# Kernel tuning notes

Hardware: AMD Instinct MI355X
Metric: run time of the kernel (lower is better)

The kernel has to match this reference:

```python
import jax, jax.numpy as jnp
import numpy as np

# Model dims (match init_kwargs)
L = 2048; B = 2; E = 1024; H = 16; NUM = 2; NG = 4; DG = 16
ODIM = E // H // NUM        # 32  origin_head_dim
DQK = ODIM * NG             # 128 qk_head_dim
QKD = DQK * H               # 2048 qk_dim
DV = E // H                 # 64  v_head_dim
EPS = 1e-12


def _one_mask(n, e, n_groups, step):
    """Faithful port of MultiheadSpluAttention.get_one_mask (numpy, setup-time only)."""
    e1 = e * n_groups
    mask = np.ones((n, e1))
    row_num = (e1 - e) // step + 1
    group1 = [list(range(i * step, i * step + e)) for i in range(row_num)]
    group2 = group1[::-1]
    group_index = [group1, group2]
    col_index = []
    l = n // row_num
    k = 0
    for i in range(l):
        for j in range(i * row_num, (i + 1) * row_num):
            col_index.append(group_index[k][j % row_num])
        k = 1 - k
    if n % row_num != 0:
        for j in range(l * row_num, n):
            col_index.append(group_index[k][j % row_num])
    mask[np.arange(n).reshape(-1, 1), np.array(col_index)] = 0
    return mask


def _build_masks(n):
    # head 0: no mask; heads 1..H-1 use step = head index
    ms = [np.zeros((n, DQK))]
    for s in range(1, H):
        ms.append(_one_mask(n, ODIM, NG, s))
    masks = np.stack(ms).astype(bool)            # (H, n, DQK); True = zero-out
    gmask = np.ones((n, DQK), dtype=bool)        # global: keep only first/last DG rows
    gmask[:DG, :] = False
    gmask[n - DG:, :] = False
    return jnp.asarray(masks), jnp.asarray(gmask)


def _xavier(key, shape, gain=1.0):
    fan_out, fan_in = shape
    a = gain * np.sqrt(6.0 / (fan_in + fan_out))
    return jax.random.uniform(key, shape, jnp.float32, -a, a)


def setup_inputs() -> dict:
    key = jax.random.key(0)
    ks = jax.random.split(key, 8)
    g = 1.0 / np.sqrt(2.0)
    masks, gmask = _build_masks(L)
    return {
        "query": jax.random.normal(ks[0], (L, B, E), jnp.float32),
        "key": jax.random.normal(ks[1], (L, B, E), jnp.float32),
        "value": jax.random.normal(ks[2], (L, B, E), jnp.float32),
        "Wq": _xavier(ks[3], (QKD, E), g), "bq": jnp.zeros((QKD,), jnp.float32),
        "Wk": _xavier(ks[4], (QKD, E), g), "bk": jnp.zeros((QKD,), jnp.float32),
        "Wv": _xavier(ks[5], (E, E), g),  "bv": jnp.zeros((E,), jnp.float32),
        "Wo": _xavier(ks[6], (E, E)),     "bo": jnp.zeros((E,), jnp.float32),
        "masks": masks,   # (H, L, DQK) bool
        "gmask": gmask,   # (L, DQK) bool
    }


def reference(query, key, value, Wq, bq, Wk, bk, Wv, bv, Wo, bo, masks, gmask):
    Lq, Bb, Ee = query.shape
    S = key.shape[0]
    Hh, _, dqk = masks.shape
    dv = Ee // Hh
    scaling = float(Wq.shape[0]) ** (-0.5)  # qk_dim ** -0.5

    q = jax.nn.relu(query @ Wq.T + bq) * scaling          # (L, B, QKD)
    k = jax.nn.relu(key @ Wk.T + bk)                       # (S, B, QKD)
    v = value @ Wv.T + bv                                  # (S, B, E)

    q = q.reshape(Lq, Bb, Hh, dqk).transpose(1, 2, 0, 3)   # (B, H, L, dqk)
    k = k.reshape(S, Bb, Hh, dqk).transpose(1, 2, 0, 3)    # (B, H, S, dqk)
    v = v.reshape(S, Bb, Hh, dv).transpose(1, 2, 0, 3)     # (B, H, S, dv)

    q1 = jnp.where(masks[None, :, :Lq], 0.0, q)            # per-head group mask
    k1 = jnp.where(masks[None, :, :S], 0.0, k)
    kg = jnp.where(gmask[None, None, :S], 0.0, k)          # keep only global tokens

    w = (jnp.einsum('bhld,bhsd->bhls', q1, k1)
         + jnp.einsum('bhld,bhsd->bhls', q, kg))           # (B, H, L, S)
    denom = jnp.maximum(jnp.sum(w, axis=-1, keepdims=True), EPS)
    w = w / denom                                          # relu-linear normalization

    out = jnp.einsum('bhls,bhsd->bhld', w, v)              # (B, H, L, dv)
    out = out.transpose(2, 0, 1, 3).reshape(Lq, Bb, Ee)    # (L, B, E)
    return out @ Wo.T + bo
```

## Files before the change

### kernel.cpp

```cpp
#include <hip/hip_runtime.h>

typedef unsigned short u16;
typedef __attribute__((ext_vector_type(8))) short s16x8;
typedef __attribute__((ext_vector_type(4))) float f32x4;

#define DEV static __device__ __forceinline__

#define CB 2
#define CM 4096
#define MBH 16640
#define OQ 0u
#define OK 4194304u
#define OV 8388608u
#define OWQ 12582912u
#define OWK 14680064u
#define OWV 16777216u
#define OWO 17825792u
#define SCALING 0.022097086912079608f

DEV float b2f(u16 u) { union { unsigned int i; float f; } x; x.i = (unsigned int)u << 16; return x.f; }
DEV u16 f2b(float f) {
  union { float f; unsigned int i; } x; x.f = f;
  unsigned int r = (x.i + 0x7FFFu + ((x.i >> 16) & 1u)) >> 16;
  return (u16)r;
}

DEV void async_cp16(const u16* g, u16* l) {
  __builtin_amdgcn_global_load_lds((__attribute__((address_space(1))) void*)g,
                                   (__attribute__((address_space(3))) void*)l,
                                   16, 0, 0);
}

#define MFMA16 __builtin_amdgcn_mfma_f32_16x16x32_bf16

__global__ void detect_stride(const unsigned char* __restrict__ m, int* __restrict__ flag) {
  if (threadIdx.x == 0) {
    const size_t base = (size_t)1 * 2048 * 128;
    int shift = 0;
    const int cands[3] = {0, 2, 3};
    for (int t = 0; t < 3; ++t) {
      int s = cands[t];
      bool ok = (m[(base + 100) << s] == 1) && (m[(base + 10) << s] == 0) &&
                (m[(base + 32) << s] == 1) && (m[(base + 31) << s] == 0);
      if (ok) { shift = s; break; }
    }
    *flag = shift;
  }
}

struct ConvDesc { const float* src; unsigned dst_off; unsigned n; };
struct ConvArgs { ConvDesc d[7]; };

__global__ __launch_bounds__(256) void convert_all(ConvArgs a, u16* __restrict__ dst_base) {
  ConvDesc dd = a.d[blockIdx.y];
  unsigned i = (blockIdx.x * 256u + threadIdx.x) * 4u;
  if (i >= dd.n) return;
  float4 v = *(const float4*)(dd.src + i);
  ushort4 p;
  p.x = f2b(v.x); p.y = f2b(v.y); p.z = f2b(v.z); p.w = f2b(v.w);
  *(ushort4*)(dst_base + dd.dst_off + i) = p;
}

__global__ __launch_bounds__(256) void gemm_qkv(const u16* __restrict__ cvt,
                                                const float* __restrict__ bq,
                                                const float* __restrict__ bk,
                                                const float* __restrict__ bv,
                                                u16* __restrict__ qbuf,
                                                u16* __restrict__ kbuf,
                                                u16* __restrict__ vbuf,
                                                u16* __restrict__ kg,
                                                const unsigned char* __restrict__ mb,
                                                const int* __restrict__ flag) {
  __shared__ u16 sA[128 * 64];
  __shared__ u16 sB[128 * 64];
  const int bx = blockIdx.x;

  const u16* A; const u16* W; const float* bias; u16* C;
  int N, nx; bool relu, domask; float scale;
  if (bx < 16) {
    A = cvt + OQ; W = cvt + OWQ; bias = bq; C = qbuf;
    N = 2048; nx = bx; relu = true; domask = false; scale = SCALING;
  } else if (bx < 32) {
    A = cvt + OK; W = cvt + OWK; bias = bk; C = kbuf;
    N = 2048; nx = bx - 16; relu = true; domask = true; scale = 1.0f;
  } else {
    A = cvt + OV; W = cvt + OWV; bias = bv; C = vbuf;
    N = 1024; nx = bx - 32; relu = false; domask = false; scale = 1.0f;
  }

  const int tid = threadIdx.x;
  const int lane = tid & 63;
  const int wv = tid >> 6;
  const int m0 = blockIdx.y * 128;
  const int n0 = nx * 128;

  const int rowi = lane >> 3;
  const int chk = lane & 7;
  const int lr = lane & 15;
  const int lq = lane >> 4;
  const int mq = (wv >> 1) * 64;
  const int nq = (wv & 1) * 64;

  const int shift = domask ? *flag : 0;

  f32x4 acc[4][4] = {};

  for (int k0 = 0; k0 < 1024; k0 += 64) {
#pragma unroll
    for (int i = 0; i < 4; ++i) {
      int t = wv * 4 + i;
      int row = t * 8 + rowi;
      async_cp16(A + (size_t)(m0 + row) * 1024 + k0 + chk * 8, sA + t * 512);
      async_cp16(W + (size_t)(n0 + row) * 1024 + k0 + chk * 8, sB + t * 512);
    }
    __syncthreads();
    s16x8 af[4][2], bfr[4][2];
#pragma unroll
    for (int mt = 0; mt < 4; ++mt) {
      af[mt][0] = *(const s16x8*)&sA[(mq + mt * 16 + lr) * 64 + lq * 8];
      af[mt][1] = *(const s16x8*)&sA[(mq + mt * 16 + lr) * 64 + 32 + lq * 8];
    }
#pragma unroll
    for (int nt = 0; nt < 4; ++nt) {
      bfr[nt][0] = *(const s16x8*)&sB[(nq + nt * 16 + lr) * 64 + lq * 8];
      bfr[nt][1] = *(const s16x8*)&sB[(nq + nt * 16 + lr) * 64 + 32 + lq * 8];
    }
#pragma unroll
    for (int kk = 0; kk < 2; ++kk)
#pragma unroll
      for (int mt = 0; mt < 4; ++mt)
#pragma unroll
        for (int nt = 0; nt < 4; ++nt)
          acc[mt][nt] = MFMA16(af[mt][kk], bfr[nt][kk], acc[mt][nt], 0, 0, 0);
    __syncthreads();
  }

#pragma unroll
  for (int mt = 0; mt < 4; ++mt) {
#pragma unroll
    for (int nt = 0; nt < 4; ++nt) {
      int col = n0 + nq + nt * 16 + lr;
      float bv_ = bias[col];
      size_t mcb = (size_t)(col >> 7) * 262144 + (col & 127);
#pragma unroll
      for (int r = 0; r < 4; ++r) {
        int row = m0 + mq + mt * 16 + lq * 4 + r;
        float x = acc[mt][nt][r] + bv_;
        if (relu) x = fmaxf(x, 0.0f);
        x *= scale;
        u16 vb = f2b(x);
        if (domask) {
          int s = row >> 1;
          u16 out = mb[(mcb + (size_t)s * 128) << shift] ? (u16)0 : vb;
          C[(size_t)row * N + col] = out;
          if (s < 16 || s >= 2032) {
            int gi = s < 16 ? s : s - 2016;
            kg[(size_t)((gi << 1) | (row & 1)) * 2048 + col] = vb;
          }
        } else {
          C[(size_t)row * N + col] = vb;
        }
      }
    }
  }
}

__global__ __launch_bounds__(256) void gemm_bt_f32(const u16* __restrict__ A,
                                                   const u16* __restrict__ W,
                                                   const float* __restrict__ bias,
                                                   float* __restrict__ Cp,
                                                   int M, int N, int K) {
  __shared__ u16 sA[128 * 64];
  __shared__ u16 sB[128 * 64];
  const int tid = threadIdx.x;
  const int lane = tid & 63;
  const int wv = tid >> 6;
  const int m0 = blockIdx.y * 128;
  const int n0 = blockIdx.x * 128;

  const int rowi = lane >> 3;
  const int chk = lane & 7;
  const int lr = lane & 15;
  const int lq = lane >> 4;
  const int mq = (wv >> 1) * 64;
  const int nq = (wv & 1) * 64;

  f32x4 acc[4][4] = {};

  for (int k0 = 0; k0 < K; k0 += 64) {
#pragma unroll
    for (int i = 0; i < 4; ++i) {
      int t = wv * 4 + i;
      int row = t * 8 + rowi;
      async_cp16(A + (size_t)(m0 + row) * K + k0 + chk * 8, sA + t * 512);
      async_cp16(W + (size_t)(n0 + row) * K + k0 + chk * 8, sB + t * 512);
    }
    __syncthreads();
    s16x8 af[4][2], bfr[4][2];
#pragma unroll
    for (int mt = 0; mt < 4; ++mt) {
      af[mt][0] = *(const s16x8*)&sA[(mq + mt * 16 + lr) * 64 + lq * 8];
      af[mt][1] = *(const s16x8*)&sA[(mq + mt * 16 + lr) * 64 + 32 + lq * 8];
    }
#pragma unroll
    for (int nt = 0; nt < 4; ++nt) {
      bfr[nt][0] = *(const s16x8*)&sB[(nq + nt * 16 + lr) * 64 + lq * 8];
      bfr[nt][1] = *(const s16x8*)&sB[(nq + nt * 16 + lr) * 64 + 32 + lq * 8];
    }
#pragma unroll
    for (int kk = 0; kk < 2; ++kk)
#pragma unroll
      for (int mt = 0; mt < 4; ++mt)
#pragma unroll
        for (int nt = 0; nt < 4; ++nt)
          acc[mt][nt] = MFMA16(af[mt][kk], bfr[nt][kk], acc[mt][nt], 0, 0, 0);
    __syncthreads();
  }

#pragma unroll
  for (int mt = 0; mt < 4; ++mt) {
#pragma unroll
    for (int nt = 0; nt < 4; ++nt) {
      int col = n0 + nq + nt * 16 + lr;
      float bv = bias[col];
#pragma unroll
      for (int r = 0; r < 4; ++r) {
        int row = m0 + mq + mt * 16 + lq * 4 + r;
        Cp[(size_t)row * N + col] = acc[mt][nt][r] + bv;
      }
    }
  }
}

__global__ __launch_bounds__(256) void build_m_mfma(const u16* __restrict__ kbuf,
                                                    const u16* __restrict__ vbuf,
                                                    const u16* __restrict__ kgbuf,
                                                    float* __restrict__ Mbuf) {
  __shared__ u16 sKr[32 * 128];
  __shared__ u16 sVr[32 * 64];
  const int tid = threadIdx.x;
  const int lane = tid & 63;
  const int wv = tid >> 6;
  const int lr = lane & 15;
  const int lq = lane >> 4;
  const int chunk = blockIdx.x;
  const int bh = blockIdx.y;
  const int b = bh >> 4, h = bh & 15;

  const int sA = wv * 4 + (lane >> 4);
  const int dA = (lane & 15) * 8;
  const int sV = wv * 8 + (lane >> 3);
  const int eV = (lane & 7) * 8;
  u16* dstK1 = sKr + wv * 512;
  u16* dstK2 = sKr + 2048 + wv * 512;
  u16* dstV = sVr + wv * 512;

  const s16x8 onesf = {0x3F80, 0x3F80, 0x3F80, 0x3F80, 0x3F80, 0x3F80, 0x3F80, 0x3F80};

  f32x4 acc[2][4] = {};
  f32x4 accm[2] = {};

  for (int ks = 0; ks < 8; ++ks) {
    const int s0 = chunk * 256 + ks * 32;
    async_cp16(kbuf + (size_t)((s0 + sA) * 2 + b) * 2048 + h * 128 + dA, dstK1);
    async_cp16(kbuf + (size_t)((s0 + 16 + sA) * 2 + b) * 2048 + h * 128 + dA, dstK2);
    async_cp16(vbuf + (size_t)((s0 + sV) * 2 + b) * 1024 + h * 64 + eV, dstV);
    __syncthreads();
    s16x8 A0, A1, B0, B1, B2, B3;
#pragma unroll
    for (int j = 0; j < 8; ++j) {
      const int sr = (lq * 8 + j) * 128;
      A0[j] = (short)sKr[sr + wv * 32 + lr];
      A1[j] = (short)sKr[sr + wv * 32 + 16 + lr];
      const int vr = (lq * 8 + j) * 64;
      B0[j] = (short)sVr[vr + lr];
      B1[j] = (short)sVr[vr + 16 + lr];
      B2[j] = (short)sVr[vr + 32 + lr];
      B3[j] = (short)sVr[vr + 48 + lr];
    }
    acc[0][0] = MFMA16(A0, B0, acc[0][0], 0, 0, 0);
    acc[0][1] = MFMA16(A0, B1, acc[0][1], 0, 0, 0);
    acc[0][2] = MFMA16(A0, B2, acc[0][2], 0, 0, 0);
    acc[0][3] = MFMA16(A0, B3, acc[0][3], 0, 0, 0);
    acc[1][0] = MFMA16(A1, B0, acc[1][0], 0, 0, 0);
    acc[1][1] = MFMA16(A1, B1, acc[1][1], 0, 0, 0);
    acc[1][2] = MFMA16(A1, B2, acc[1][2], 0, 0, 0);
    acc[1][3] = MFMA16(A1, B3, acc[1][3], 0, 0, 0);
    accm[0] = MFMA16(A0, onesf, accm[0], 0, 0, 0);
    accm[1] = MFMA16(A1, onesf, accm[1], 0, 0, 0);
    __syncthreads();
  }

  float* Mg = Mbuf + (size_t)bh * MBH;
#pragma unroll
  for (int dg = 0; dg < 2; ++dg) {
    const int dbase = wv * 32 + dg * 16 + lq * 4;
#pragma unroll
    for (int eg = 0; eg < 4; ++eg)
#pragma unroll
      for (int r = 0; r < 4; ++r)
        atomicAdd(&Mg[(size_t)(dbase + r) * 64 + eg * 16 + lr], acc[dg][eg][r]);
    if (lr == 0) {
#pragma unroll
      for (int r = 0; r < 4; ++r) atomicAdd(&Mg[16384 + dbase + r], accm[dg][r]);
    }
  }

  if (chunk == 0) {
    f32x4 acc2[2][4] = {};
    f32x4 accm2[2] = {};
    const int sVact = sV < 16 ? sV : 2016 + sV;
    async_cp16(kgbuf + (size_t)(sA * 2 + b) * 2048 + h * 128 + dA, dstK1);
    async_cp16(kgbuf + (size_t)((16 + sA) * 2 + b) * 2048 + h * 128 + dA, dstK2);
    async_cp16(vbuf + (size_t)(sVact * 2 + b) * 1024 + h * 64 + eV, dstV);
    __syncthreads();
    s16x8 A0, A1, B0, B1, B2, B3;
#pragma unroll
    for (int j = 0; j < 8; ++j) {
      const int sr = (lq * 8 + j) * 128;
      A0[j] = (short)sKr[sr + wv * 32 + lr];
      A1[j] = (short)sKr[sr + wv * 32 + 16 + lr];
      const int vr = (lq * 8 + j) * 64;
      B0[j] = (short)sVr[vr + lr];
      B1[j] = (short)sVr[vr + 16 + lr];
      B2[j] = (short)sVr[vr + 32 + lr];
      B3[j] = (short)sVr[vr + 48 + lr];
    }
    acc2[0][0] = MFMA16(A0, B0, acc2[0][0], 0, 0, 0);
    acc2[0][1] = MFMA16(A0, B1, acc2[0][1], 0, 0, 0);
    acc2[0][2] = MFMA16(A0, B2, acc2[0][2], 0, 0, 0);
    acc2[0][3] = MFMA16(A0, B3, acc2[0][3], 0, 0, 0);
    acc2[1][0] = MFMA16(A1, B0, acc2[1][0], 0, 0, 0);
    acc2[1][1] = MFMA16(A1, B1, acc2[1][1], 0, 0, 0);
    acc2[1][2] = MFMA16(A1, B2, acc2[1][2], 0, 0, 0);
    acc2[1][3] = MFMA16(A1, B3, acc2[1][3], 0, 0, 0);
    accm2[0] = MFMA16(A0, onesf, accm2[0], 0, 0, 0);
    accm2[1] = MFMA16(A1, onesf, accm2[1], 0, 0, 0);
#pragma unroll
    for (int dg = 0; dg < 2; ++dg) {
      const int dbase = wv * 32 + dg * 16 + lq * 4;
#pragma unroll
      for (int eg = 0; eg < 4; ++eg)
#pragma unroll
        for (int r = 0; r < 4; ++r)
          Mg[8192 + (size_t)(dbase + r) * 64 + eg * 16 + lr] = acc2[dg][eg][r];
      if (lr == 0) {
#pragma unroll
        for (int r = 0; r < 4; ++r) Mg[16512 + dbase + r] = accm2[dg][r];
      }
    }
  }
}

__global__ __launch_bounds__(128) void prep_m(const float* __restrict__ Mbuf,
                                              u16* __restrict__ Mp) {
  const int n = blockIdx.x;
  const int bh = blockIdx.y;
  const int d = threadIdx.x;
  const float* Mg = Mbuf + (size_t)bh * MBH;
  float v1 = 0.f, v2 = 0.f;
  if (n < 64) { v1 = Mg[d * 64 + n]; v2 = Mg[8192 + d * 64 + n]; }
  else if (n == 64) { v1 = Mg[16384 + d]; v2 = Mg[16512 + d]; }
  u16 h1 = f2b(v1); float l1 = v1 - b2f(h1);
  u16 h2 = f2b(v2); float l2 = v2 - b2f(h2);
  u16* dst = Mp + (size_t)bh * 40960;
  const int dsw = d ^ ((n & 7) << 3);
  dst[(0 * 80 + n) * 128 + dsw] = h1;
  dst[(1 * 80 + n) * 128 + dsw] = f2b(l1);
  dst[(2 * 80 + n) * 128 + dsw] = h2;
  dst[(3 * 80 + n) * 128 + dsw] = f2b(l2);
}

__global__ __launch_bounds__(256) void apply_mfma(const u16* __restrict__ qbuf,
                                                  const u16* __restrict__ Mp,
                                                  u16* __restrict__ attn,
                                                  const unsigned char* __restrict__ mb,
                                                  const int* __restrict__ flag) {
  __shared__ u16 sB[4 * 80 * 128];
  const int tid = threadIdx.x;
  const int lane = tid & 63;
  const int wv = tid >> 6;
  const int lr = lane & 15;
  const int lq = lane >> 4;
  const int bh = blockIdx.x;
  const int b = bh >> 4, h = bh & 15;
  const int l0 = blockIdx.y * 256;
  const int shift = *flag;

  {
    const u16* src = Mp + (size_t)bh * 40960;
#pragma unroll
    for (int i = 0; i < 20; ++i)
      async_cp16(src + (size_t)(i * 4 + wv) * 512 + lane * 8, sB + (i * 4 + wv) * 512);
  }
  __syncthreads();

  f32x4 acc[4][5] = {};
  const int lrow = l0 + wv * 64;

  for (int d0 = 0; d0 < 128; d0 += 32) {
    s16x8 aq[4], a1[4];
#pragma unroll
    for (int mt = 0; mt < 4; ++mt) {
      const int l = lrow + mt * 16 + lr;
      aq[mt] = *(const s16x8*)&qbuf[((size_t)(l * 2 + b)) * 2048 + h * 128 + d0 + lq * 8];
      const size_t mi = ((size_t)(h * 2048 + l)) * 128 + d0 + lq * 8;
      s16x8 t = aq[mt];
      if (shift == 0) {
        unsigned long long mm = *(const unsigned long long*)&mb[mi];
#pragma unroll
        for (int j = 0; j < 8; ++j)
          if ((mm >> (8 * j)) & 0xffull) t[j] = 0;
      } else {
#pragma unroll
        for (int j = 0; j < 8; ++j)
          if (mb[(mi + j) << shift]) t[j] = 0;
      }
      a1[mt] = t;
    }
    const int eb = (d0 >> 3) + lq;
#pragma unroll
    for (int nt = 0; nt < 5; ++nt) {
      const int n = nt * 16 + lr;
      const u16* bp = &sB[(size_t)n * 128 + ((eb ^ (n & 7)) << 3)];
      s16x8 b1h = *(const s16x8*)&bp[0];
      s16x8 b1l = *(const s16x8*)&bp[10240];
      s16x8 b2h = *(const s16x8*)&bp[20480];
      s16x8 b2l = *(const s16x8*)&bp[30720];
#pragma unroll
      for (int mt = 0; mt < 4; ++mt) {
        acc[mt][nt] = MFMA16(a1[mt], b1h, acc[mt][nt], 0, 0, 0);
        acc[mt][nt] = MFMA16(a1[mt], b1l, acc[mt][nt], 0, 0, 0);
        acc[mt][nt] = MFMA16(aq[mt], b2h, acc[mt][nt], 0, 0, 0);
        acc[mt][nt] = MFMA16(aq[mt], b2l, acc[mt][nt], 0, 0, 0);
      }
    }
  }

#pragma unroll
  for (int mt = 0; mt < 4; ++mt) {
#pragma unroll
    for (int r = 0; r < 4; ++r) {
      float den = __shfl(acc[mt][4][r], lane & 48);
      float inv = 1.0f / fmaxf(den, 1e-12f);
      const int row = lrow + mt * 16 + lq * 4 + r;
      u16* o = attn + ((size_t)(row * 2 + b)) * 1024 + h * 64;
#pragma unroll
      for (int nt = 0; nt < 4; ++nt)
        o[nt * 16 + lr] = f2b(acc[mt][nt][r] * inv);
    }
  }
}

extern "C" void kernel_launch(void* const* d_in, const int* in_sizes, int n_in,
                              void* d_out, int out_size, void* d_ws, size_t ws_size,
                              hipStream_t stream) {
  (void)in_sizes; (void)n_in; (void)out_size; (void)ws_size;

  const float* bq = (const float*)d_in[4];
  const float* bk = (const float*)d_in[6];
  const float* bv = (const float*)d_in[8];
  const float* bo = (const float*)d_in[10];
  const unsigned char* mbytes = (const unsigned char*)d_in[11];

  char* ws = (char*)d_ws;
  u16* qbuf = (u16*)ws;
  u16* kbuf = (u16*)(ws + 16777216);
  float* Mbuf = (float*)(ws + 33554432);
  int* flag = (int*)(ws + 35684352);
  u16* cvt = (u16*)(ws + 35684368);
  u16* vbuf = (u16*)d_out;
  u16* kgbuf = (u16*)((char*)d_out + 8388608);
  u16* Mprep = (u16*)d_out;
  u16* attn = kbuf;

  hipMemsetAsync(Mbuf, 0, 32 * MBH * sizeof(float), stream);
  detect_stride<<<dim3(1), dim3(64), 0, stream>>>(mbytes, flag);

  ConvArgs ca;
  ca.d[0] = {(const float*)d_in[0], OQ, 4194304u};
  ca.d[1] = {(const float*)d_in[1], OK, 4194304u};
  ca.d[2] = {(const float*)d_in[2], OV, 4194304u};
  ca.d[3] = {(const float*)d_in[3], OWQ, 2097152u};
  ca.d[4] = {(const float*)d_in[5], OWK, 2097152u};
  ca.d[5] = {(const float*)d_in[7], OWV, 1048576u};
  ca.d[6] = {(const float*)d_in[9], OWO, 1048576u};
  convert_all<<<dim3(4096, 7), dim3(256), 0, stream>>>(ca, cvt);

  dim3 blk(256);
  gemm_qkv<<<dim3(40, 32), blk, 0, stream>>>(cvt, bq, bk, bv, qbuf, kbuf, vbuf, kgbuf, mbytes, flag);
  build_m_mfma<<<dim3(8, 32), blk, 0, stream>>>(kbuf, vbuf, kgbuf, Mbuf);
  prep_m<<<dim3(80, 32), dim3(128), 0, stream>>>(Mbuf, Mprep);
  apply_mfma<<<dim3(32, 8), blk, 0, stream>>>(qbuf, Mprep, attn, mbytes, flag);
  gemm_bt_f32<<<dim3(8, 32), blk, 0, stream>>>(attn, cvt + OWO, bo, (float*)d_out, CM, 1024, 1024);
}
```

Baseline: 349.8 us.

## Rewrite QKV projection GEMM as 256x256 tiled, double-buffered, XOR-swizzled pipelined kernel

Replaces the 128x128 single-buffered QKV GEMM with a 512-thread kernel that computes 256x256 output tiles using eight waves. Shared-memory tiles are double-buffered and XOR-swizzled, and global loads for upcoming k-steps are interleaved with MFMA phases under fine-grained barriers and s_setprio. The goal is to hide load latency, avoid LDS bank conflicts and raise data reuse per load. In exchange there are fewer blocks (320), so the grid may fill the GPU less evenly, and register and LDS pressure goes up.

```diff
diff --git a/kernel.cpp b/kernel.cpp
--- a/kernel.cpp
+++ b/kernel.cpp
@@ -61,104 +61,135 @@
   *(ushort4*)(dst_base + dd.dst_off + i) = p;
 }
 
-__global__ __launch_bounds__(256) void gemm_qkv(const u16* __restrict__ cvt,
-                                                const float* __restrict__ bq,
-                                                const float* __restrict__ bk,
-                                                const float* __restrict__ bv,
-                                                u16* __restrict__ qbuf,
-                                                u16* __restrict__ kbuf,
-                                                u16* __restrict__ vbuf,
-                                                u16* __restrict__ kg,
-                                                const unsigned char* __restrict__ mb,
-                                                const int* __restrict__ flag) {
-  __shared__ u16 sA[128 * 64];
-  __shared__ u16 sB[128 * 64];
+__global__ __launch_bounds__(512, 2) void gemm_qkv8(const u16* __restrict__ cvt,
+                                                    const float* __restrict__ bq,
+                                                    const float* __restrict__ bk,
+                                                    const float* __restrict__ bv,
+                                                    u16* __restrict__ qbuf,
+                                                    u16* __restrict__ kbuf,
+                                                    u16* __restrict__ vbuf,
+                                                    u16* __restrict__ kg,
+                                                    const unsigned char* __restrict__ mb,
+                                                    const int* __restrict__ flag) {
+  __shared__ u16 sL[2][4][8192];
   const int bx = blockIdx.x;
 
   const u16* A; const u16* W; const float* bias; u16* C;
   int N, nx; bool relu, domask; float scale;
-  if (bx < 16) {
+  if (bx < 8) {
     A = cvt + OQ; W = cvt + OWQ; bias = bq; C = qbuf;
     N = 2048; nx = bx; relu = true; domask = false; scale = SCALING;
-  } else if (bx < 32) {
+  } else if (bx < 16) {
     A = cvt + OK; W = cvt + OWK; bias = bk; C = kbuf;
-    N = 2048; nx = bx - 16; relu = true; domask = true; scale = 1.0f;
+    N = 2048; nx = bx - 8; relu = true; domask = true; scale = 1.0f;
   } else {
     A = cvt + OV; W = cvt + OWV; bias = bv; C = vbuf;
-    N = 1024; nx = bx - 32; relu = false; domask = false; scale = 1.0f;
+    N = 1024; nx = bx - 16; relu = false; domask = false; scale = 1.0f;
   }
 
   const int tid = threadIdx.x;
   const int lane = tid & 63;
-  const int wv = tid >> 6;
-  const int m0 = blockIdx.y * 128;
-  const int n0 = nx * 128;
-
-  const int rowi = lane >> 3;
-  const int chk = lane & 7;
+  const int wid = tid >> 6;
+  const int m0 = blockIdx.y * 256;
+  const int n0 = nx * 256;
   const int lr = lane & 15;
   const int lq = lane >> 4;
-  const int mq = (wv >> 1) * 64;
-  const int nq = (wv & 1) * 64;
+  const int wqr = wid >> 2;
+  const int wqc = wid & 3;
+  const int growL = (wid << 3) + (lane >> 3);
+  const int gcol = ((lane & 7) ^ (lane >> 3)) << 3;
 
   const int shift = domask ? *flag : 0;
 
-  f32x4 acc[4][4] = {};
-
-  for (int k0 = 0; k0 < 1024; k0 += 64) {
-#pragma unroll
-    for (int i = 0; i < 4; ++i) {
-      int t = wv * 4 + i;
-      int row = t * 8 + rowi;
-      async_cp16(A + (size_t)(m0 + row) * 1024 + k0 + chk * 8, sA + t * 512);
-      async_cp16(W + (size_t)(n0 + row) * 1024 + k0 + chk * 8, sB + t * 512);
-    }
-    __syncthreads();
-    s16x8 af[4][2], bfr[4][2];
-#pragma unroll
-    for (int mt = 0; mt < 4; ++mt) {
-      af[mt][0] = *(const s16x8*)&sA[(mq + mt * 16 + lr) * 64 + lq * 8];
-      af[mt][1] = *(const s16x8*)&sA[(mq + mt * 16 + lr) * 64 + 32 + lq * 8];
-    }
-#pragma unroll
-    for (int nt = 0; nt < 4; ++nt) {
-      bfr[nt][0] = *(const s16x8*)&sB[(nq + nt * 16 + lr) * 64 + lq * 8];
-      bfr[nt][1] = *(const s16x8*)&sB[(nq + nt * 16 + lr) * 64 + 32 + lq * 8];
-    }
-#pragma unroll
-    for (int kk = 0; kk < 2; ++kk)
-#pragma unroll
-      for (int mt = 0; mt < 4; ++mt)
-#pragma unroll
-        for (int nt = 0; nt < 4; ++nt)
-          acc[mt][nt] = MFMA16(af[mt][kk], bfr[nt][kk], acc[mt][nt], 0, 0, 0);
-    __syncthreads();
-  }
-
-#pragma unroll
-  for (int mt = 0; mt < 4; ++mt) {
-#pragma unroll
-    for (int nt = 0; nt < 4; ++nt) {
-      int col = n0 + nq + nt * 16 + lr;
-      float bv_ = bias[col];
-      size_t mcb = (size_t)(col >> 7) * 262144 + (col & 127);
-#pragma unroll
-      for (int r = 0; r < 4; ++r) {
-        int row = m0 + mq + mt * 16 + lq * 4 + r;
-        float x = acc[mt][nt][r] + bv_;
-        if (relu) x = fmaxf(x, 0.0f);
-        x *= scale;
-        u16 vb = f2b(x);
-        if (domask) {
-          int s = row >> 1;
-          u16 out = mb[(mcb + (size_t)s * 128) << shift] ? (u16)0 : vb;
-          C[(size_t)row * N + col] = out;
-          if (s < 16 || s >= 2032) {
-            int gi = s < 16 ? s : s - 2016;
-            kg[(size_t)((gi << 1) | (row & 1)) * 2048 + col] = vb;
+#define STG(TH, Q)                                                                        \
+  do {                                                                                    \
+    const u16* _b = (Q) < 2 ? A : W;                                                      \
+    const int _r0 = ((Q) < 2 ? m0 + (Q) * 128 : n0 + ((Q) - 2) * 128) + growL;            \
+    async_cp16(_b + (size_t)_r0 * 1024 + (TH) * 64 + gcol, &sL[(TH) & 1][Q][wid * 512]);  \
+    async_cp16(_b + (size_t)(_r0 + 64) * 1024 + (TH) * 64 + gcol,                         \
+               &sL[(TH) & 1][Q][(wid + 8) * 512]);                                        \
+  } while (0)
+
+#define PHS(P, MH, NH)                                                                    \
+  {                                                                                       \
+    s16x8 afr[4][2], bfr[2][2];                                                           \
+    _Pragma("unroll") for (int mt = 0; mt < 4; ++mt)                                      \
+        _Pragma("unroll") for (int kk = 0; kk < 2; ++kk)                                  \
+            afr[mt][kk] = *(const s16x8*)&sL[bufo][MH][(wqr * 64 + mt * 16 + lr) * 64 +   \
+                                                      (((kk * 4 + lq) ^ (lr & 7)) << 3)]; \
+    _Pragma("unroll") for (int nt = 0; nt < 2; ++nt)                                      \
+        _Pragma("unroll") for (int kk = 0; kk < 2; ++kk)                                  \
+            bfr[nt][kk] = *(const s16x8*)&sL[bufo][2 + NH][(wqc * 32 + nt * 16 + lr) * 64 + \
+                                                      (((kk * 4 + lq) ^ (lr & 7)) << 3)]; \
+    __builtin_amdgcn_s_setprio(1);                                                        \
+    _Pragma("unroll") for (int mt = 0; mt < 4; ++mt)                                      \
+        _Pragma("unroll") for (int nt = 0; nt < 2; ++nt) {                                \
+          acc[P][mt][nt] = MFMA16(afr[mt][0], bfr[nt][0], acc[P][mt][nt], 0, 0, 0);       \
+          acc[P][mt][nt] = MFMA16(afr[mt][1], bfr[nt][1], acc[P][mt][nt], 0, 0, 0);       \
+        }                                                                                 \
+    __builtin_amdgcn_s_setprio(0);                                                        \
+  }
+
+  f32x4 acc[4][4][2] = {};
+
+  STG(0, 0); STG(0, 2); STG(0, 3); STG(0, 1); STG(1, 0); STG(1, 2);
+  asm volatile("s_waitcnt vmcnt(4)" ::: "memory");
+  __builtin_amdgcn_s_barrier();
+
+  for (int t = 0; t < 16; ++t) {
+    const int bufo = t & 1;
+    if (t + 1 < 16) STG(t + 1, 3);
+    PHS(0, 0, 0)
+    __builtin_amdgcn_s_barrier();
+    if (t + 1 < 16) STG(t + 1, 1);
+    PHS(1, 0, 1)
+    __builtin_amdgcn_s_barrier();
+    __builtin_amdgcn_sched_barrier(0);
+    if (t + 2 < 16) STG(t + 2, 0);
+    PHS(2, 1, 0)
+    __builtin_amdgcn_s_barrier();
+    __builtin_amdgcn_sched_barrier(0);
+    if (t + 2 < 16) STG(t + 2, 2);
+    PHS(3, 1, 1)
+    if (t < 14) {
+      asm volatile("s_waitcnt vmcnt(4)" ::: "memory");
+      __builtin_amdgcn_s_barrier();
+    } else if (t == 14) {
+      asm volatile("s_waitcnt vmcnt(0)" ::: "memory");
+      __builtin_amdgcn_s_barrier();
+    }
+  }
+#undef PHS
+#undef STG
+
+#pragma unroll
+  for (int p = 0; p < 4; ++p) {
+    const int mh = p >> 1, nh = p & 1;
+#pragma unroll
+    for (int nt = 0; nt < 2; ++nt) {
+      const int col = n0 + nh * 128 + wqc * 32 + nt * 16 + lr;
+      const float bv_ = bias[col];
+      const size_t mcb = (size_t)(col >> 7) * 262144 + (col & 127);
+#pragma unroll
+      for (int mt = 0; mt < 4; ++mt) {
+#pragma unroll
+        for (int r = 0; r < 4; ++r) {
+          const int row = m0 + mh * 128 + wqr * 64 + mt * 16 + lq * 4 + r;
+          float x = acc[p][mt][nt][r] + bv_;
+          if (relu) x = fmaxf(x, 0.0f);
+          x *= scale;
+          u16 vbb = f2b(x);
+          if (domask) {
+            int s = row >> 1;
+            u16 out = mb[(mcb + (size_t)s * 128) << shift] ? (u16)0 : vbb;
+            C[(size_t)row * N + col] = out;
+            if (s < 16 || s >= 2032) {
+              int gi = s < 16 ? s : s - 2016;
+              kg[(size_t)((gi << 1) | (row & 1)) * 2048 + col] = vbb;
+            }
+          } else {
+            C[(size_t)row * N + col] = vbb;
           }
-        } else {
-          C[(size_t)row * N + col] = vb;
         }
       }
     }
@@ -487,10 +518,9 @@
   ca.d[6] = {(const float*)d_in[9], OWO, 1048576u};
   convert_all<<<dim3(4096, 7), dim3(256), 0, stream>>>(ca, cvt);
 
-  dim3 blk(256);
-  gemm_qkv<<<dim3(40, 32), blk, 0, stream>>>(cvt, bq, bk, bv, qbuf, kbuf, vbuf, kgbuf, mbytes, flag);
-  build_m_mfma<<<dim3(8, 32), blk, 0, stream>>>(kbuf, vbuf, kgbuf, Mbuf);
+  gemm_qkv8<<<dim3(20, 16), dim3(512), 0, stream>>>(cvt, bq, bk, bv, qbuf, kbuf, vbuf, kgbuf, mbytes, flag);
+  build_m_mfma<<<dim3(8, 32), dim3(256), 0, stream>>>(kbuf, vbuf, kgbuf, Mbuf);
   prep_m<<<dim3(80, 32), dim3(128), 0, stream>>>(Mbuf, Mprep);
-  apply_mfma<<<dim3(32, 8), blk, 0, stream>>>(qbuf, Mprep, attn, mbytes, flag);
-  gemm_bt_f32<<<dim3(8, 32), blk, 0, stream>>>(attn, cvt + OWO, bo, (float*)d_out, CM, 1024, 1024);
-}
+  apply_mfma<<<dim3(32, 8), dim3(256), 0, stream>>>(qbuf, Mprep, attn, mbytes, flag);
+  gemm_bt_f32<<<dim3(8, 32), dim3(256), 0, stream>>>(attn, cvt + OWO, bo, (float*)d_out, CM, 1024, 1024);
+}
```

Measured after the change: 338.7 us. 1.03x faster.
